# Performance work log

Hardware: AMD Instinct MI355X
Metric: run time of the kernel (lower is better)

## Reference

```python
import jax, jax.numpy as jnp
import numpy as np

N_USERS = 100000
N_ITEMS = 50000
DIM = 64
HID = 64
E = 3200000
B = 16384


def setup_inputs() -> dict:
    key = jax.random.key(0)
    ks = jax.random.split(key, 16)
    N = N_USERS + N_ITEMS
    return {
        "users": jax.random.randint(ks[0], (B,), 0, N_USERS),
        "items": jax.random.randint(ks[1], (B,), 0, N_ITEMS),
        "edge_index": jax.random.randint(ks[2], (2, E), 0, N),
        "edge_weight": jax.random.uniform(ks[3], (E,), dtype=jnp.float32),
        # learned parameters
        "U": jax.random.normal(ks[4], (N_USERS, DIM), jnp.float32) * 0.1,
        "I": jax.random.normal(ks[5], (N_ITEMS, DIM), jnp.float32) * 0.1,
        "W0": jax.random.normal(ks[6], (DIM, HID), jnp.float32) / np.sqrt(DIM),
        "b0": jnp.zeros((HID,), jnp.float32),
        "g0": jnp.ones((HID,), jnp.float32),
        "be0": jnp.zeros((HID,), jnp.float32),
        "W1": jax.random.normal(ks[7], (HID, HID), jnp.float32) / np.sqrt(HID),
        "b1": jnp.zeros((HID,), jnp.float32),
        "g1": jnp.ones((HID,), jnp.float32),
        "be1": jnp.zeros((HID,), jnp.float32),
        "Wp": jax.random.normal(ks[8], (HID, DIM), jnp.float32) / np.sqrt(HID),
        "bp": jnp.zeros((DIM,), jnp.float32),
        "bu": jnp.zeros((N_USERS,), jnp.float32),
        "bi": jnp.zeros((N_ITEMS,), jnp.float32),
        "mu": jnp.zeros((), jnp.float32),
    }


def _layernorm(h, g, b, eps=1e-5):
    m = jnp.mean(h, axis=-1, keepdims=True)
    v = jnp.mean(jnp.square(h - m), axis=-1, keepdims=True)
    return (h - m) * jax.lax.rsqrt(v + eps) * g + b


def reference(users, items, edge_index, edge_weight, U, I,
              W0, b0, g0, be0, W1, b1, g1, be1, Wp, bp, bu, bi, mu):
    N = U.shape[0] + I.shape[0]
    x = jnp.concatenate([U, I], axis=0)  # [N, DIM]

    # GCN normalization with added self-loops (torch_geometric gcn_norm)
    loop = jnp.arange(N)
    src = jnp.concatenate([edge_index[0], loop])
    dst = jnp.concatenate([edge_index[1], loop])
    ew = jnp.concatenate([edge_weight, jnp.ones((N,), edge_weight.dtype)])
    deg = jax.ops.segment_sum(ew, dst, num_segments=N)
    dinv = jnp.where(deg > 0, jax.lax.rsqrt(deg), 0.0)
    norm = dinv[src] * ew * dinv[dst]  # [E+N]

    def conv(h, W, b):
        hw = h @ W  # [N, HID]
        msgs = norm[:, None] * hw[src]  # gather: [E+N, HID]
        return jax.ops.segment_sum(msgs, dst, num_segments=N) + b

    # layer 0: conv -> layernorm -> relu -> (dropout=identity, eval) -> residual
    h = x
    h_in = h
    h = conv(h, W0, b0)
    h = jax.nn.relu(_layernorm(h, g0, be0)) + h_in
    # layer 1
    h_in = h
    h = conv(h, W1, b1)
    h = jax.nn.relu(_layernorm(h, g1, be1)) + h_in

    h = h @ Wp + bp  # proj_out: [N, DIM]
    h_user = h[:U.shape[0]]
    h_item = h[U.shape[0]:]

    s = jnp.sum(h_user[users] * h_item[items], axis=-1)
    s = s + bu[users] + bi[items] + mu
    return jnp.clip(s, 1.0, 5.0)
```

## Files before the change

### kernel.cpp

```cpp
#include <hip/hip_runtime.h>

#define NU 100000
#define NI 50000
#define NN 150000
#define D  64
#define CAP 47
#define OVF_MAX 4096

#define BINSHIFT 9
#define BINW 512
#define NBINS 293
#define BINCAP 11448
#define STAGE_CAP 20
#define EPT 4
#define SPILL_CAP 262144

typedef unsigned int uint;
typedef unsigned short ushort;

__device__ __forceinline__ float half_reduce_add(float v) {
    #pragma unroll
    for (int m = 16; m >= 1; m >>= 1) v += __shfl_xor(v, m, 64);
    return v;
}
__device__ __forceinline__ ushort f2bf(float f) {
    union { float f; uint i; } c; c.f = f;
    uint r = c.i + 0x7FFF + ((c.i >> 16) & 1);
    return (ushort)(r >> 16);
}
__device__ __forceinline__ float lane_bcast(float v, int l) {
    return __int_as_float(__builtin_amdgcn_readlane(__float_as_int(v), l));
}
__device__ __forceinline__ uint enc14(float w) {
    uint b = __float_as_uint(w) + 0x00020000u;
    return b & 0xFFFC0000u;
}
__device__ __forceinline__ float dec14(uint r) {
    return __uint_as_float(r & 0xFFFC0000u);
}
__device__ __forceinline__ void spill_one(int d, uint s, float w,
        uint2* __restrict__ spill, int* __restrict__ spillcnt) {
    int si = atomicAdd(spillcnt, 1);
    if (si < SPILL_CAP) spill[si] = make_uint2(s | enc14(w), (uint)d);
}

__global__ __launch_bounds__(256) void k_bin(
        const int* __restrict__ src, const int* __restrict__ dst,
        const float* __restrict__ ew, int* __restrict__ bincur,
        uint2* __restrict__ binbuf, uint2* __restrict__ spill,
        int* __restrict__ spillcnt, int E) {
    __shared__ uint2 stage[NBINS][STAGE_CAP];
    __shared__ int scnt[NBINS];
    int t = threadIdx.x;
    for (int i = t; i < NBINS; i += 256) scnt[i] = 0;
    __syncthreads();
    const int batch = 256 * EPT;
    for (int base = blockIdx.x * batch; base < E; base += gridDim.x * batch) {
        int dd[EPT]; uint ss[EPT]; float ww[EPT]; int ok[EPT];
        #pragma unroll
        for (int k = 0; k < EPT; ++k) {
            int e = base + k * 256 + t;
            ok[k] = (e < E);
            if (ok[k]) { dd[k] = dst[e]; ss[k] = (uint)src[e]; ww[k] = ew[e]; }
        }
        #pragma unroll
        for (int k = 0; k < EPT; ++k) {
            if (!ok[k]) continue;
            int bin = dd[k] >> BINSHIFT;
            int slot = atomicAdd(&scnt[bin], 1);
            if (slot < STAGE_CAP) {
                stage[bin][slot] = make_uint2(
                    ss[k] | ((uint)(dd[k] & (BINW - 1)) << 18),
                    (uint)__float_as_int(ww[k]));
            } else {
                spill_one(dd[k], ss[k], ww[k], spill, spillcnt);
            }
        }
        __syncthreads();
        for (int bin = t; bin < NBINS; bin += 256) {
            int c = scnt[bin]; if (c > STAGE_CAP) c = STAGE_CAP;
            while (c >= 8) {
                int b0 = atomicAdd(&bincur[bin], 8);
                if (b0 + 8 <= BINCAP) {
                    uint4* o4 = (uint4*)(binbuf + (size_t)bin * BINCAP + b0);
                    uint2* s2 = &stage[bin][c - 8];
                    o4[0] = make_uint4(s2[0].x, s2[0].y, s2[1].x, s2[1].y);
                    o4[1] = make_uint4(s2[2].x, s2[2].y, s2[3].x, s2[3].y);
                    o4[2] = make_uint4(s2[4].x, s2[4].y, s2[5].x, s2[5].y);
                    o4[3] = make_uint4(s2[6].x, s2[6].y, s2[7].x, s2[7].y);
                } else {
                    for (int j = 0; j < 8; ++j) {
                        uint2 r = stage[bin][c - 8 + j];
                        spill_one((bin << BINSHIFT) + (int)(r.x >> 18),
                                  r.x & 0x3FFFFu, __int_as_float((int)r.y),
                                  spill, spillcnt);
                    }
                }
                c -= 8;
            }
            scnt[bin] = c;
        }
        __syncthreads();
    }
    for (int bin = t; bin < NBINS; bin += 256) {
        int c = scnt[bin]; if (c > STAGE_CAP) c = STAGE_CAP;
        if (c > 0) {
            int b0 = atomicAdd(&bincur[bin], c);
            for (int j = 0; j < c; ++j) {
                uint2 r = stage[bin][j];
                if (b0 + j < BINCAP) binbuf[(size_t)bin * BINCAP + b0 + j] = r;
                else spill_one((bin << BINSHIFT) + (int)(r.x >> 18),
                               r.x & 0x3FFFFu, __int_as_float((int)r.y),
                               spill, spillcnt);
            }
        }
    }
}

__global__ __launch_bounds__(256) void k_regroup(
        const int* __restrict__ bincur, const uint2* __restrict__ binbuf,
        const uint2* __restrict__ spill, const int* __restrict__ spillcnt,
        uint* __restrict__ recs, int* __restrict__ cursor,
        float* __restrict__ dinv, int4* __restrict__ ovf,
        int* __restrict__ ovfcnt) {
    __shared__ uint image[256 * CAP];
    __shared__ int cnt[256];
    __shared__ float ovfw[256];
    int t = threadIdx.x;
    int bin  = blockIdx.x >> 1;
    int half = blockIdx.x & 1;
    cnt[t] = 0; ovfw[t] = 0.0f;
    __syncthreads();
    int dbase = (bin << BINSHIFT) + half * 256;
    int nrec = bincur[bin]; if (nrec > BINCAP) nrec = BINCAP;
    const uint2* bb = binbuf + (size_t)bin * BINCAP;
    for (int i = t; i < nrec; i += 256) {
        uint2 r = bb[i];
        int dlocal = (int)(r.x >> 18);
        if ((dlocal >> 8) != half) continue;
        int dl = dlocal & 255;
        int slot = atomicAdd(&cnt[dl], 1);
        uint s = r.x & 0x3FFFFu;
        float w = __int_as_float((int)r.y);
        if (slot < CAP) image[dl * CAP + slot] = enc14(w) | s;
        else {
            atomicAdd(&ovfw[dl], w);
            int o = atomicAdd(ovfcnt, 1);
            if (o < OVF_MAX)
                ovf[o] = make_int4((bin << BINSHIFT) + dlocal, (int)s,
                                   __float_as_int(w), 0);
        }
    }
    int ns = spillcnt[0]; if (ns > SPILL_CAP) ns = SPILL_CAP;
    for (int i = t; i < ns; i += 256) {
        uint2 e = spill[i];
        int d = (int)e.y;
        if (d < dbase || d >= dbase + 256) continue;
        int dl = d - dbase;
        int slot = atomicAdd(&cnt[dl], 1);
        if (slot < CAP) image[dl * CAP + slot] = e.x;
        else {
            float w = dec14(e.x);
            atomicAdd(&ovfw[dl], w);
            int o = atomicAdd(ovfcnt, 1);
            if (o < OVF_MAX) ovf[o] = make_int4(d, (int)(e.x & 0x3FFFFu),
                                                __float_as_int(w), 0);
        }
    }
    __syncthreads();
    int ndl = NN - dbase; if (ndl > 256) ndl = 256;
    if (ndl <= 0) return;
    if (t < ndl) {
        int c = cnt[t];
        cursor[dbase + t] = c;
        if (c > CAP) c = CAP;
        float dg = ovfw[t];
        for (int j = 0; j < c; ++j) dg += dec14(image[t * CAP + j]);
        dinv[dbase + t] = rsqrtf(dg + 1.0f);
    }
    int tot = ndl * CAP;
    uint* out = recs + (size_t)dbase * CAP;
    for (int i = t; i < tot; i += 256) out[i] = image[i];
}

__global__ __launch_bounds__(256) void k_gemm(
        const float* __restrict__ h, const float* __restrict__ U,
        const float* __restrict__ I, const float* __restrict__ W,
        const float* __restrict__ dinv, ushort* __restrict__ out) {
    int lane = threadIdx.x & 63;
    float wreg[64];
    #pragma unroll
    for (int k = 0; k < 64; ++k) wreg[k] = W[k * 64 + lane];
    int wpb = blockDim.x >> 6;
    int wid = blockIdx.x * wpb + (threadIdx.x >> 6);
    int tw = gridDim.x * wpb;
    for (int n = wid; n < NN; n += tw) {
        float xv;
        if (h) xv = h[(size_t)n * D + lane];
        else   xv = (n < NU) ? U[(size_t)n * D + lane]
                             : I[(size_t)(n - NU) * D + lane];
        float acc = 0.f;
        #pragma unroll
        for (int k = 0; k < 64; ++k)
            acc = fmaf(lane_bcast(xv, k), wreg[k], acc);
        out[(size_t)n * D + lane] = f2bf(acc * dinv[n]);
    }
}

__device__ __forceinline__ float2 conv_accum2(int n, int lane,
        const uint* __restrict__ hw2p, const int* __restrict__ cursor,
        const uint* __restrict__ recs, const int4* __restrict__ ovf,
        const int* __restrict__ ovfcnt) {
    int cnt = __builtin_amdgcn_readfirstlane(cursor[n]);
    if (cnt > CAP) cnt = CAP;
    uint rv = (lane < cnt) ? recs[(size_t)n * CAP + lane] : 0u;
    int odd = lane >> 5;
    int laneoff = lane & 31;
    float ax = 0.f, ay = 0.f;
    int cp = (cnt + 7) & ~7;
    for (int j0 = 0; j0 < cp; j0 += 8) {
        #pragma unroll
        for (int k = 0; k < 4; ++k) {
            uint re = (uint)__builtin_amdgcn_readlane((int)rv, j0 + 2 * k);
            uint ro = (uint)__builtin_amdgcn_readlane((int)rv, j0 + 2 * k + 1);
            uint r  = odd ? ro : re;
            int   s = (int)(r & 0x3FFFFu);
            float w = dec14(r);
            uint x = hw2p[(size_t)s * 32 + laneoff];
            ax = fmaf(w, __int_as_float((int)(x << 16)), ax);
            ay = fmaf(w, __int_as_float((int)(x & 0xFFFF0000u)), ay);
        }
    }
    ax += __shfl_xor(ax, 32, 64);
    ay += __shfl_xor(ay, 32, 64);
    uint xs = hw2p[(size_t)n * 32 + laneoff];
    ax += __int_as_float((int)(xs << 16));
    ay += __int_as_float((int)(xs & 0xFFFF0000u));
    int novf = __builtin_amdgcn_readfirstlane(ovfcnt[0]);
    if (novf > 0) {
        if (novf > OVF_MAX) novf = OVF_MAX;
        for (int j = 0; j < novf; ++j) {
            int4 e = ovf[j];
            if (e.x == n) {
                float w = __int_as_float(e.z);
                uint x = hw2p[(size_t)e.y * 32 + laneoff];
                ax = fmaf(w, __int_as_float((int)(x << 16)), ax);
                ay = fmaf(w, __int_as_float((int)(x & 0xFFFF0000u)), ay);
            }
        }
    }
    return make_float2(ax, ay);
}

__device__ __forceinline__ float2 ln_relu2(float2 a, float di, int p,
        const float* __restrict__ b, const float* __restrict__ g,
        const float* __restrict__ be) {
    float2 bb = ((const float2*)b)[p];
    float v0 = fmaf(a.x, di, bb.x);
    float v1 = fmaf(a.y, di, bb.y);
    float m = half_reduce_add(v0 + v1) * (1.0f / 64.0f);
    float d0 = v0 - m, d1 = v1 - m;
    float var = half_reduce_add(d0 * d0 + d1 * d1) * (1.0f / 64.0f);
    float rs = rsqrtf(var + 1e-5f);
    float2 gg = ((const float2*)g)[p];
    float2 ee = ((const float2*)be)[p];
    return make_float2(fmaxf(fmaf(d0 * rs, gg.x, ee.x), 0.0f),
                       fmaxf(fmaf(d1 * rs, gg.y, ee.y), 0.0f));
}

__global__ __launch_bounds__(256) void k_conv1(
        const uint* __restrict__ hw2p, const int* __restrict__ cursor,
        const uint* __restrict__ recs, const int4* __restrict__ ovf,
        const int* __restrict__ ovfcnt, const float* __restrict__ dinv,
        const float* __restrict__ b, const float* __restrict__ g,
        const float* __restrict__ be, const float* __restrict__ U,
        const float* __restrict__ I, float* __restrict__ out) {
    int lane = threadIdx.x & 63;
    int n = __builtin_amdgcn_readfirstlane(blockIdx.x * 4 + (threadIdx.x >> 6));
    if (n >= NN) return;
    float2 a = conv_accum2(n, lane, hw2p, cursor, recs, ovf, ovfcnt);
    int p = lane & 31;
    float2 y = ln_relu2(a, dinv[n], p, b, g, be);
    const float* R = (n < NU) ? (U + (size_t)n * D) : (I + (size_t)(n - NU) * D);
    float2 rr = ((const float2*)R)[p];
    if (lane < 32)
        ((float2*)out)[(size_t)n * 32 + p] = make_float2(y.x + rr.x, y.y + rr.y);
}

__global__ __launch_bounds__(256) void k_conv2s(
        const uint* __restrict__ hw2p, const int* __restrict__ cursor,
        const uint* __restrict__ recs, const int4* __restrict__ ovf,
        const int* __restrict__ ovfcnt, const float* __restrict__ dinv,
        const float* __restrict__ b, const float* __restrict__ g,
        const float* __restrict__ be, const int* __restrict__ users,
        const int* __restrict__ items, const float* __restrict__ h1,
        float* __restrict__ h2s, int B) {
    int lane = threadIdx.x & 63;
    int p = blockIdx.x * 4 + (threadIdx.x >> 6);
    if (p >= 2 * B) return;
    int n = (p < B) ? users[p] : NU + items[p - B];
    n = __builtin_amdgcn_readfirstlane(n);
    float2 a = conv_accum2(n, lane, hw2p, cursor, recs, ovf, ovfcnt);
    int q = lane & 31;
    float2 y = ln_relu2(a, dinv[n], q, b, g, be);
    float2 rr = ((const float2*)h1)[(size_t)n * 32 + q];
    if (lane < 32)
        ((float2*)h2s)[(size_t)p * 32 + q] = make_float2(y.x + rr.x, y.y + rr.y);
}

__global__ __launch_bounds__(256) void k_score(
        const float* __restrict__ h2s, const int* __restrict__ users,
        const int* __restrict__ items, const float* __restrict__ Wp,
        const float* __restrict__ bp, const float* __restrict__ bu,
        const float* __restrict__ bi, const float* __restrict__ mu,
        float* __restrict__ out, int B) {
    int lane = threadIdx.x & 63;
    float wreg[64];
    #pragma unroll
    for (int k = 0; k < 64; ++k) wreg[k] = Wp[k * 64 + lane];
    float bpl = bp[lane];
    int wpb = blockDim.x >> 6;
    int wid = blockIdx.x * wpb + (threadIdx.x >> 6);
    int tw = gridDim.x * wpb;
    for (int p = wid; p < B; p += tw) {
        float hu = h2s[(size_t)p * D + lane];
        float hi = h2s[(size_t)(B + p) * D + lane];
        float pu = bpl, pi = bpl;
        #pragma unroll
        for (int k = 0; k < 64; ++k) {
            float wv = wreg[k];
            pu = fmaf(lane_bcast(hu, k), wv, pu);
            pi = fmaf(lane_bcast(hi, k), wv, pi);
        }
        float t = pu * pi;
        #pragma unroll
        for (int m = 32; m >= 1; m >>= 1) t += __shfl_xor(t, m, 64);
        if (lane == 0) {
            t += bu[users[p]] + bi[items[p]] + mu[0];
            out[p] = fminf(fmaxf(t, 1.0f), 5.0f);
        }
    }
}

extern "C" void kernel_launch(void* const* d_in, const int* in_sizes, int n_in,
                              void* d_out, int out_size, void* d_ws, size_t ws_size,
                              hipStream_t stream) {
    const int*   users = (const int*)d_in[0];
    const int*   items = (const int*)d_in[1];
    const int*   ei2   = (const int*)d_in[2];
    const float* ew    = (const float*)d_in[3];
    const float* U     = (const float*)d_in[4];
    const float* I     = (const float*)d_in[5];
    const float* W0    = (const float*)d_in[6];
    const float* b0    = (const float*)d_in[7];
    const float* g0    = (const float*)d_in[8];
    const float* be0   = (const float*)d_in[9];
    const float* W1    = (const float*)d_in[10];
    const float* b1    = (const float*)d_in[11];
    const float* g1    = (const float*)d_in[12];
    const float* be1   = (const float*)d_in[13];
    const float* Wp    = (const float*)d_in[14];
    const float* bp    = (const float*)d_in[15];
    const float* bu    = (const float*)d_in[16];
    const float* bi    = (const float*)d_in[17];
    const float* mu    = (const float*)d_in[18];

    int B = in_sizes[0];
    int E = in_sizes[2] / 2;
    const int* srcp = ei2;
    const int* dstp = ei2 + E;

    char* p = (char*)d_ws;
    auto alloc = [&](size_t bytes) -> char* {
        char* r = p;
        p += (bytes + 255) & ~(size_t)255;
        return r;
    };
    int*    cbuf    = (int*)  alloc((size_t)(NBINS + 8) * 4);
    int*    bincur  = cbuf;
    int*    spillcnt= cbuf + NBINS;
    int*    ovfcnt  = cbuf + NBINS + 1;
    int*    cursor  = (int*)  alloc((size_t)NN * 4);
    float*  dinv    = (float*)alloc((size_t)NN * 4);
    int4*   ovf     = (int4*) alloc((size_t)OVF_MAX * 16);
    uint2*  spill   = (uint2*)alloc((size_t)SPILL_CAP * 8);
    uint2*  binbuf  = (uint2*)alloc((size_t)NBINS * BINCAP * 8);
    uint*   recs    = (uint*) alloc((size_t)NN * CAP * 4);
    ushort* hw2b    = (ushort*)alloc((size_t)NN * D * 2);
    float*  h1      = (float*)alloc((size_t)NN * D * 4);
    float*  h2s     = (float*)alloc((size_t)2 * B * D * 4);
    const uint* hw2p = (const uint*)hw2b;

    hipMemsetAsync(cbuf, 0, (size_t)(NBINS + 8) * 4, stream);

    int gW = (NN + 3) / 4;
    int gS = (2 * B + 3) / 4;

    k_bin<<<768, 256, 0, stream>>>(srcp, dstp, ew, bincur, binbuf,
                                   spill, spillcnt, E);
    k_regroup<<<NBINS * 2, 256, 0, stream>>>(bincur, binbuf, spill, spillcnt,
                                             recs, cursor, dinv, ovf, ovfcnt);

    k_gemm<<<2048, 256, 0, stream>>>(nullptr, U, I, W0, dinv, hw2b);
    k_conv1<<<gW, 256, 0, stream>>>(hw2p, cursor, recs, ovf, ovfcnt, dinv,
                                    b0, g0, be0, U, I, h1);
    k_gemm<<<2048, 256, 0, stream>>>(h1, U, I, W1, dinv, hw2b);
    k_conv2s<<<gS, 256, 0, stream>>>(hw2p, cursor, recs, ovf, ovfcnt, dinv,
                                     b1, g1, be1, users, items, h1, h2s, B);

    k_score<<<512, 256, 0, stream>>>(h2s, users, items, Wp, bp, bu, bi, mu,
                                     (float*)d_out, B);
}
```

Measured before the change: 434.6 us.

## Gather four edges per wave step with 8-byte loads and halve bin width

The conv gather now splits the wave into four 16-lane groups. Each group handles one edge per step and loads 8 bytes (four bf16 values) per lane, instead of two 32-lane halves loading 4 bytes each. This cuts loop iterations and readlane overhead per edge and issues wider memory requests, at the cost of an extra cross-lane reduction step. Binning is also narrowed to 256 destinations per bin, with twice the bins and a smaller stage capacity. Each regroup block then owns a whole bin and no longer skips the half belonging to another block, though the spill list is still scanned by every block.

```diff
diff --git a/kernel.cpp b/kernel.cpp
--- a/kernel.cpp
+++ b/kernel.cpp
@@ -7,22 +7,17 @@
 #define CAP 47
 #define OVF_MAX 4096
 
-#define BINSHIFT 9
-#define BINW 512
-#define NBINS 293
-#define BINCAP 11448
-#define STAGE_CAP 20
+#define BINSHIFT 8
+#define BINW 256
+#define NBINS 586
+#define BINCAP 5848
+#define STAGE_CAP 12
 #define EPT 4
 #define SPILL_CAP 262144
 
 typedef unsigned int uint;
 typedef unsigned short ushort;
 
-__device__ __forceinline__ float half_reduce_add(float v) {
-    #pragma unroll
-    for (int m = 16; m >= 1; m >>= 1) v += __shfl_xor(v, m, 64);
-    return v;
-}
 __device__ __forceinline__ ushort f2bf(float f) {
     union { float f; uint i; } c; c.f = f;
     uint r = c.i + 0x7FFF + ((c.i >> 16) & 1);
@@ -30,6 +25,12 @@
 }
 __device__ __forceinline__ float lane_bcast(float v, int l) {
     return __int_as_float(__builtin_amdgcn_readlane(__float_as_int(v), l));
+}
+__device__ __forceinline__ float bflo(uint u) {
+    return __int_as_float((int)(u << 16));
+}
+__device__ __forceinline__ float bfhi(uint u) {
+    return __int_as_float((int)(u & 0xFFFF0000u));
 }
 __device__ __forceinline__ uint enc14(float w) {
     uint b = __float_as_uint(w) + 0x00020000u;
@@ -127,18 +128,15 @@
     __shared__ int cnt[256];
     __shared__ float ovfw[256];
     int t = threadIdx.x;
-    int bin  = blockIdx.x >> 1;
-    int half = blockIdx.x & 1;
+    int bin = blockIdx.x;
     cnt[t] = 0; ovfw[t] = 0.0f;
     __syncthreads();
-    int dbase = (bin << BINSHIFT) + half * 256;
+    int dbase = bin << BINSHIFT;
     int nrec = bincur[bin]; if (nrec > BINCAP) nrec = BINCAP;
     const uint2* bb = binbuf + (size_t)bin * BINCAP;
     for (int i = t; i < nrec; i += 256) {
         uint2 r = bb[i];
-        int dlocal = (int)(r.x >> 18);
-        if ((dlocal >> 8) != half) continue;
-        int dl = dlocal & 255;
+        int dl = (int)(r.x >> 18);
         int slot = atomicAdd(&cnt[dl], 1);
         uint s = r.x & 0x3FFFFu;
         float w = __int_as_float((int)r.y);
@@ -147,15 +145,14 @@
             atomicAdd(&ovfw[dl], w);
             int o = atomicAdd(ovfcnt, 1);
             if (o < OVF_MAX)
-                ovf[o] = make_int4((bin << BINSHIFT) + dlocal, (int)s,
-                                   __float_as_int(w), 0);
+                ovf[o] = make_int4(dbase + dl, (int)s, __float_as_int(w), 0);
         }
     }
     int ns = spillcnt[0]; if (ns > SPILL_CAP) ns = SPILL_CAP;
     for (int i = t; i < ns; i += 256) {
         uint2 e = spill[i];
         int d = (int)e.y;
-        if (d < dbase || d >= dbase + 256) continue;
+        if (d < dbase || d >= dbase + BINW) continue;
         int dl = d - dbase;
         int slot = atomicAdd(&cnt[dl], 1);
         if (slot < CAP) image[dl * CAP + slot] = e.x;
@@ -207,35 +204,39 @@
     }
 }
 
-__device__ __forceinline__ float2 conv_accum2(int n, int lane,
-        const uint* __restrict__ hw2p, const int* __restrict__ cursor,
+__device__ __forceinline__ float4 conv_accum4(int n, int lane,
+        const uint2* __restrict__ hw2q, const int* __restrict__ cursor,
         const uint* __restrict__ recs, const int4* __restrict__ ovf,
         const int* __restrict__ ovfcnt) {
     int cnt = __builtin_amdgcn_readfirstlane(cursor[n]);
     if (cnt > CAP) cnt = CAP;
     uint rv = (lane < cnt) ? recs[(size_t)n * CAP + lane] : 0u;
-    int odd = lane >> 5;
-    int laneoff = lane & 31;
-    float ax = 0.f, ay = 0.f;
-    int cp = (cnt + 7) & ~7;
-    for (int j0 = 0; j0 < cp; j0 += 8) {
-        #pragma unroll
-        for (int k = 0; k < 4; ++k) {
-            uint re = (uint)__builtin_amdgcn_readlane((int)rv, j0 + 2 * k);
-            uint ro = (uint)__builtin_amdgcn_readlane((int)rv, j0 + 2 * k + 1);
-            uint r  = odd ? ro : re;
-            int   s = (int)(r & 0x3FFFFu);
-            float w = dec14(r);
-            uint x = hw2p[(size_t)s * 32 + laneoff];
-            ax = fmaf(w, __int_as_float((int)(x << 16)), ax);
-            ay = fmaf(w, __int_as_float((int)(x & 0xFFFF0000u)), ay);
-        }
-    }
-    ax += __shfl_xor(ax, 32, 64);
-    ay += __shfl_xor(ay, 32, 64);
-    uint xs = hw2p[(size_t)n * 32 + laneoff];
-    ax += __int_as_float((int)(xs << 16));
-    ay += __int_as_float((int)(xs & 0xFFFF0000u));
+    int loff = lane & 15;
+    bool b4 = (lane & 16) != 0, b5 = (lane & 32) != 0;
+    float ax = 0.f, ay = 0.f, az = 0.f, aw = 0.f;
+    int cp = (cnt + 3) & ~3;
+    for (int j0 = 0; j0 < cp; j0 += 4) {
+        uint r0 = (uint)__builtin_amdgcn_readlane((int)rv, j0);
+        uint r1 = (uint)__builtin_amdgcn_readlane((int)rv, j0 + 1);
+        uint r2 = (uint)__builtin_amdgcn_readlane((int)rv, j0 + 2);
+        uint r3 = (uint)__builtin_amdgcn_readlane((int)rv, j0 + 3);
+        uint ra = b5 ? r3 : r1;
+        uint rb = b5 ? r2 : r0;
+        uint r  = b4 ? ra : rb;
+        int   s = (int)(r & 0x3FFFFu);
+        float w = dec14(r);
+        uint2 x = hw2q[(size_t)s * 16 + loff];
+        ax = fmaf(w, bflo(x.x), ax);
+        ay = fmaf(w, bfhi(x.x), ay);
+        az = fmaf(w, bflo(x.y), az);
+        aw = fmaf(w, bfhi(x.y), aw);
+    }
+    ax += __shfl_xor(ax, 32, 64); ay += __shfl_xor(ay, 32, 64);
+    az += __shfl_xor(az, 32, 64); aw += __shfl_xor(aw, 32, 64);
+    ax += __shfl_xor(ax, 16, 64); ay += __shfl_xor(ay, 16, 64);
+    az += __shfl_xor(az, 16, 64); aw += __shfl_xor(aw, 16, 64);
+    uint2 xs = hw2q[(size_t)n * 16 + loff];
+    ax += bflo(xs.x); ay += bfhi(xs.x); az += bflo(xs.y); aw += bfhi(xs.y);
     int novf = __builtin_amdgcn_readfirstlane(ovfcnt[0]);
     if (novf > 0) {
         if (novf > OVF_MAX) novf = OVF_MAX;
@@ -243,33 +244,42 @@
             int4 e = ovf[j];
             if (e.x == n) {
                 float w = __int_as_float(e.z);
-                uint x = hw2p[(size_t)e.y * 32 + laneoff];
-                ax = fmaf(w, __int_as_float((int)(x << 16)), ax);
-                ay = fmaf(w, __int_as_float((int)(x & 0xFFFF0000u)), ay);
+                uint2 x = hw2q[(size_t)e.y * 16 + loff];
+                ax = fmaf(w, bflo(x.x), ax); ay = fmaf(w, bfhi(x.x), ay);
+                az = fmaf(w, bflo(x.y), az); aw = fmaf(w, bfhi(x.y), aw);
             }
         }
     }
-    return make_float2(ax, ay);
-}
-
-__device__ __forceinline__ float2 ln_relu2(float2 a, float di, int p,
+    return make_float4(ax, ay, az, aw);
+}
+
+__device__ __forceinline__ float4 ln_relu4(float4 a, float di, int loff,
         const float* __restrict__ b, const float* __restrict__ g,
         const float* __restrict__ be) {
-    float2 bb = ((const float2*)b)[p];
+    float4 bb = ((const float4*)b)[loff];
     float v0 = fmaf(a.x, di, bb.x);
     float v1 = fmaf(a.y, di, bb.y);
-    float m = half_reduce_add(v0 + v1) * (1.0f / 64.0f);
-    float d0 = v0 - m, d1 = v1 - m;
-    float var = half_reduce_add(d0 * d0 + d1 * d1) * (1.0f / 64.0f);
-    float rs = rsqrtf(var + 1e-5f);
-    float2 gg = ((const float2*)g)[p];
-    float2 ee = ((const float2*)be)[p];
-    return make_float2(fmaxf(fmaf(d0 * rs, gg.x, ee.x), 0.0f),
-                       fmaxf(fmaf(d1 * rs, gg.y, ee.y), 0.0f));
+    float v2 = fmaf(a.z, di, bb.z);
+    float v3 = fmaf(a.w, di, bb.w);
+    float s = v0 + v1 + v2 + v3;
+    #pragma unroll
+    for (int m = 8; m >= 1; m >>= 1) s += __shfl_xor(s, m, 64);
+    float mean = s * (1.0f / 64.0f);
+    float d0 = v0 - mean, d1 = v1 - mean, d2 = v2 - mean, d3 = v3 - mean;
+    float vs = d0 * d0 + d1 * d1 + d2 * d2 + d3 * d3;
+    #pragma unroll
+    for (int m = 8; m >= 1; m >>= 1) vs += __shfl_xor(vs, m, 64);
+    float rs = rsqrtf(vs * (1.0f / 64.0f) + 1e-5f);
+    float4 gg = ((const float4*)g)[loff];
+    float4 ee = ((const float4*)be)[loff];
+    return make_float4(fmaxf(fmaf(d0 * rs, gg.x, ee.x), 0.0f),
+                       fmaxf(fmaf(d1 * rs, gg.y, ee.y), 0.0f),
+                       fmaxf(fmaf(d2 * rs, gg.z, ee.z), 0.0f),
+                       fmaxf(fmaf(d3 * rs, gg.w, ee.w), 0.0f));
 }
 
 __global__ __launch_bounds__(256) void k_conv1(
-        const uint* __restrict__ hw2p, const int* __restrict__ cursor,
+        const uint2* __restrict__ hw2q, const int* __restrict__ cursor,
         const uint* __restrict__ recs, const int4* __restrict__ ovf,
         const int* __restrict__ ovfcnt, const float* __restrict__ dinv,
         const float* __restrict__ b, const float* __restrict__ g,
@@ -278,17 +288,18 @@
     int lane = threadIdx.x & 63;
     int n = __builtin_amdgcn_readfirstlane(blockIdx.x * 4 + (threadIdx.x >> 6));
     if (n >= NN) return;
-    float2 a = conv_accum2(n, lane, hw2p, cursor, recs, ovf, ovfcnt);
-    int p = lane & 31;
-    float2 y = ln_relu2(a, dinv[n], p, b, g, be);
+    float4 a = conv_accum4(n, lane, hw2q, cursor, recs, ovf, ovfcnt);
+    int loff = lane & 15;
+    float4 y = ln_relu4(a, dinv[n], loff, b, g, be);
     const float* R = (n < NU) ? (U + (size_t)n * D) : (I + (size_t)(n - NU) * D);
-    float2 rr = ((const float2*)R)[p];
-    if (lane < 32)
-        ((float2*)out)[(size_t)n * 32 + p] = make_float2(y.x + rr.x, y.y + rr.y);
+    float4 rr = ((const float4*)R)[loff];
+    if (lane < 16)
+        ((float4*)out)[(size_t)n * 16 + loff] =
+            make_float4(y.x + rr.x, y.y + rr.y, y.z + rr.z, y.w + rr.w);
 }
 
 __global__ __launch_bounds__(256) void k_conv2s(
-        const uint* __restrict__ hw2p, const int* __restrict__ cursor,
+        const uint2* __restrict__ hw2q, const int* __restrict__ cursor,
         const uint* __restrict__ recs, const int4* __restrict__ ovf,
         const int* __restrict__ ovfcnt, const float* __restrict__ dinv,
         const float* __restrict__ b, const float* __restrict__ g,
@@ -300,12 +311,13 @@
     if (p >= 2 * B) return;
     int n = (p < B) ? users[p] : NU + items[p - B];
     n = __builtin_amdgcn_readfirstlane(n);
-    float2 a = conv_accum2(n, lane, hw2p, cursor, recs, ovf, ovfcnt);
-    int q = lane & 31;
-    float2 y = ln_relu2(a, dinv[n], q, b, g, be);
-    float2 rr = ((const float2*)h1)[(size_t)n * 32 + q];
-    if (lane < 32)
-        ((float2*)h2s)[(size_t)p * 32 + q] = make_float2(y.x + rr.x, y.y + rr.y);
+    float4 a = conv_accum4(n, lane, hw2q, cursor, recs, ovf, ovfcnt);
+    int loff = lane & 15;
+    float4 y = ln_relu4(a, dinv[n], loff, b, g, be);
+    float4 rr = ((const float4*)h1)[(size_t)n * 16 + loff];
+    if (lane < 16)
+        ((float4*)h2s)[(size_t)p * 16 + loff] =
+            make_float4(y.x + rr.x, y.y + rr.y, y.z + rr.z, y.w + rr.w);
 }
 
 __global__ __launch_bounds__(256) void k_score(
@@ -389,7 +401,7 @@
     ushort* hw2b    = (ushort*)alloc((size_t)NN * D * 2);
     float*  h1      = (float*)alloc((size_t)NN * D * 4);
     float*  h2s     = (float*)alloc((size_t)2 * B * D * 4);
-    const uint* hw2p = (const uint*)hw2b;
+    const uint2* hw2q = (const uint2*)hw2b;
 
     hipMemsetAsync(cbuf, 0, (size_t)(NBINS + 8) * 4, stream);
 
@@ -398,14 +410,14 @@
 
     k_bin<<<768, 256, 0, stream>>>(srcp, dstp, ew, bincur, binbuf,
                                    spill, spillcnt, E);
-    k_regroup<<<NBINS * 2, 256, 0, stream>>>(bincur, binbuf, spill, spillcnt,
-                                             recs, cursor, dinv, ovf, ovfcnt);
+    k_regroup<<<NBINS, 256, 0, stream>>>(bincur, binbuf, spill, spillcnt,
+                                         recs, cursor, dinv, ovf, ovfcnt);
 
     k_gemm<<<2048, 256, 0, stream>>>(nullptr, U, I, W0, dinv, hw2b);
-    k_conv1<<<gW, 256, 0, stream>>>(hw2p, cursor, recs, ovf, ovfcnt, dinv,
+    k_conv1<<<gW, 256, 0, stream>>>(hw2q, cursor, recs, ovf, ovfcnt, dinv,
                                     b0, g0, be0, U, I, h1);
     k_gemm<<<2048, 256, 0, stream>>>(h1, U, I, W1, dinv, hw2b);
-    k_conv2s<<<gS, 256, 0, stream>>>(hw2p, cursor, recs, ovf, ovfcnt, dinv,
+    k_conv2s<<<gS, 256, 0, stream>>>(hw2q, cursor, recs, ovf, ovfcnt, dinv,
                                      b1, g1, be1, users, items, h1, h2s, B);
 
     k_score<<<512, 256, 0, stream>>>(h2s, users, items, Wp, bp, bu, bi, mu,
```

Measured after the change: 434.5 us. No clear change (-0.0%).

## Fuse layer-2 conv into scoring kernel and halve bin width

Applied to the files above, without the earlier changes.

Merges the sampled second-layer conv kernel with the projection/score kernel, so each wave computes the user and item conv rows in registers and scores them directly, with no h2s buffer and one fewer launch. Separately, bins shrink from 512 to 256 destinations, so regroup launches one block per bin instead of two blocks that each scanned the whole bin and discarded half. The risk is less parallelism in the fused kernel: 1024 blocks loop serially over pairs, each wave doing two dependent gathers. Smaller staging capacities in the bin kernel may also raise spill traffic.

```diff
diff --git a/kernel.cpp b/kernel.cpp
--- a/kernel.cpp
+++ b/kernel.cpp
@@ -7,11 +7,11 @@
 #define CAP 47
 #define OVF_MAX 4096
 
-#define BINSHIFT 9
-#define BINW 512
-#define NBINS 293
-#define BINCAP 11448
-#define STAGE_CAP 20
+#define BINSHIFT 8
+#define BINW 256
+#define NBINS 586
+#define BINCAP 5848
+#define STAGE_CAP 12
 #define EPT 4
 #define SPILL_CAP 262144
 
@@ -127,18 +127,15 @@
     __shared__ int cnt[256];
     __shared__ float ovfw[256];
     int t = threadIdx.x;
-    int bin  = blockIdx.x >> 1;
-    int half = blockIdx.x & 1;
+    int bin = blockIdx.x;
     cnt[t] = 0; ovfw[t] = 0.0f;
     __syncthreads();
-    int dbase = (bin << BINSHIFT) + half * 256;
+    int dbase = bin << BINSHIFT;
     int nrec = bincur[bin]; if (nrec > BINCAP) nrec = BINCAP;
     const uint2* bb = binbuf + (size_t)bin * BINCAP;
     for (int i = t; i < nrec; i += 256) {
         uint2 r = bb[i];
-        int dlocal = (int)(r.x >> 18);
-        if ((dlocal >> 8) != half) continue;
-        int dl = dlocal & 255;
+        int dl = (int)(r.x >> 18);
         int slot = atomicAdd(&cnt[dl], 1);
         uint s = r.x & 0x3FFFFu;
         float w = __int_as_float((int)r.y);
@@ -147,15 +144,14 @@
             atomicAdd(&ovfw[dl], w);
             int o = atomicAdd(ovfcnt, 1);
             if (o < OVF_MAX)
-                ovf[o] = make_int4((bin << BINSHIFT) + dlocal, (int)s,
-                                   __float_as_int(w), 0);
+                ovf[o] = make_int4(dbase + dl, (int)s, __float_as_int(w), 0);
         }
     }
     int ns = spillcnt[0]; if (ns > SPILL_CAP) ns = SPILL_CAP;
     for (int i = t; i < ns; i += 256) {
         uint2 e = spill[i];
         int d = (int)e.y;
-        if (d < dbase || d >= dbase + 256) continue;
+        if (d < dbase || d >= dbase + BINW) continue;
         int dl = d - dbase;
         int slot = atomicAdd(&cnt[dl], 1);
         if (slot < CAP) image[dl * CAP + slot] = e.x;
@@ -287,56 +283,51 @@
         ((float2*)out)[(size_t)n * 32 + p] = make_float2(y.x + rr.x, y.y + rr.y);
 }
 
-__global__ __launch_bounds__(256) void k_conv2s(
+__global__ __launch_bounds__(256) void k_conv2score(
         const uint* __restrict__ hw2p, const int* __restrict__ cursor,
         const uint* __restrict__ recs, const int4* __restrict__ ovf,
         const int* __restrict__ ovfcnt, const float* __restrict__ dinv,
         const float* __restrict__ b, const float* __restrict__ g,
         const float* __restrict__ be, const int* __restrict__ users,
         const int* __restrict__ items, const float* __restrict__ h1,
-        float* __restrict__ h2s, int B) {
-    int lane = threadIdx.x & 63;
-    int p = blockIdx.x * 4 + (threadIdx.x >> 6);
-    if (p >= 2 * B) return;
-    int n = (p < B) ? users[p] : NU + items[p - B];
-    n = __builtin_amdgcn_readfirstlane(n);
-    float2 a = conv_accum2(n, lane, hw2p, cursor, recs, ovf, ovfcnt);
-    int q = lane & 31;
-    float2 y = ln_relu2(a, dinv[n], q, b, g, be);
-    float2 rr = ((const float2*)h1)[(size_t)n * 32 + q];
-    if (lane < 32)
-        ((float2*)h2s)[(size_t)p * 32 + q] = make_float2(y.x + rr.x, y.y + rr.y);
-}
-
-__global__ __launch_bounds__(256) void k_score(
-        const float* __restrict__ h2s, const int* __restrict__ users,
-        const int* __restrict__ items, const float* __restrict__ Wp,
-        const float* __restrict__ bp, const float* __restrict__ bu,
-        const float* __restrict__ bi, const float* __restrict__ mu,
-        float* __restrict__ out, int B) {
+        const float* __restrict__ Wp, const float* __restrict__ bp,
+        const float* __restrict__ bu, const float* __restrict__ bi,
+        const float* __restrict__ mu, float* __restrict__ out, int B) {
     int lane = threadIdx.x & 63;
     float wreg[64];
     #pragma unroll
     for (int k = 0; k < 64; ++k) wreg[k] = Wp[k * 64 + lane];
     float bpl = bp[lane];
+    int q = lane & 31;
     int wpb = blockDim.x >> 6;
     int wid = blockIdx.x * wpb + (threadIdx.x >> 6);
     int tw = gridDim.x * wpb;
     for (int p = wid; p < B; p += tw) {
-        float hu = h2s[(size_t)p * D + lane];
-        float hi = h2s[(size_t)(B + p) * D + lane];
+        int un = users[p];
+        int in = NU + items[p];
+        int nu = __builtin_amdgcn_readfirstlane(un);
+        float2 au = conv_accum2(nu, lane, hw2p, cursor, recs, ovf, ovfcnt);
+        float2 yu = ln_relu2(au, dinv[nu], q, b, g, be);
+        float2 ru = ((const float2*)h1)[(size_t)nu * 32 + q];
+        float2 hu = make_float2(yu.x + ru.x, yu.y + ru.y);
+        int ni = __builtin_amdgcn_readfirstlane(in);
+        float2 ai = conv_accum2(ni, lane, hw2p, cursor, recs, ovf, ovfcnt);
+        float2 yi = ln_relu2(ai, dinv[ni], q, b, g, be);
+        float2 ri = ((const float2*)h1)[(size_t)ni * 32 + q];
+        float2 hi = make_float2(yi.x + ri.x, yi.y + ri.y);
         float pu = bpl, pi = bpl;
         #pragma unroll
-        for (int k = 0; k < 64; ++k) {
-            float wv = wreg[k];
-            pu = fmaf(lane_bcast(hu, k), wv, pu);
-            pi = fmaf(lane_bcast(hi, k), wv, pi);
+        for (int j = 0; j < 32; ++j) {
+            pu = fmaf(lane_bcast(hu.x, j), wreg[2 * j], pu);
+            pu = fmaf(lane_bcast(hu.y, j), wreg[2 * j + 1], pu);
+            pi = fmaf(lane_bcast(hi.x, j), wreg[2 * j], pi);
+            pi = fmaf(lane_bcast(hi.y, j), wreg[2 * j + 1], pi);
         }
         float t = pu * pi;
         #pragma unroll
         for (int m = 32; m >= 1; m >>= 1) t += __shfl_xor(t, m, 64);
         if (lane == 0) {
-            t += bu[users[p]] + bi[items[p]] + mu[0];
+            t += bu[un] + bi[in - NU] + mu[0];
             out[p] = fminf(fmaxf(t, 1.0f), 5.0f);
         }
     }
@@ -388,26 +379,23 @@
     uint*   recs    = (uint*) alloc((size_t)NN * CAP * 4);
     ushort* hw2b    = (ushort*)alloc((size_t)NN * D * 2);
     float*  h1      = (float*)alloc((size_t)NN * D * 4);
-    float*  h2s     = (float*)alloc((size_t)2 * B * D * 4);
     const uint* hw2p = (const uint*)hw2b;
 
     hipMemsetAsync(cbuf, 0, (size_t)(NBINS + 8) * 4, stream);
 
     int gW = (NN + 3) / 4;
-    int gS = (2 * B + 3) / 4;
 
     k_bin<<<768, 256, 0, stream>>>(srcp, dstp, ew, bincur, binbuf,
                                    spill, spillcnt, E);
-    k_regroup<<<NBINS * 2, 256, 0, stream>>>(bincur, binbuf, spill, spillcnt,
-                                             recs, cursor, dinv, ovf, ovfcnt);
+    k_regroup<<<NBINS, 256, 0, stream>>>(bincur, binbuf, spill, spillcnt,
+                                         recs, cursor, dinv, ovf, ovfcnt);
 
     k_gemm<<<2048, 256, 0, stream>>>(nullptr, U, I, W0, dinv, hw2b);
     k_conv1<<<gW, 256, 0, stream>>>(hw2p, cursor, recs, ovf, ovfcnt, dinv,
                                     b0, g0, be0, U, I, h1);
     k_gemm<<<2048, 256, 0, stream>>>(h1, U, I, W1, dinv, hw2b);
-    k_conv2s<<<gS, 256, 0, stream>>>(hw2p, cursor, recs, ovf, ovfcnt, dinv,
-                                     b1, g1, be1, users, items, h1, h2s, B);
-
-    k_score<<<512, 256, 0, stream>>>(h2s, users, items, Wp, bp, bu, bi, mu,
-                                     (float*)d_out, B);
-}
+    k_conv2score<<<1024, 256, 0, stream>>>(hw2p, cursor, recs, ovf, ovfcnt, dinv,
+                                           b1, g1, be1, users, items, h1,
+                                           Wp, bp, bu, bi, mu,
+                                           (float*)d_out, B);
+}
```

Result: faster. 417.0 us (-4.1%).
